# Performance work log

Hardware: AMD Instinct MI355X
Metric: run time of the kernel (lower is better)

Reference implementation:

```python
import jax, jax.numpy as jnp
import numpy as np

B, N, CQ, CKV, CP = 4, 1024, 128, 64, 16
H, NB = 4, 3
D = CQ // H  # 32 per-head dim
NQ, NK = 32, 128
CENTRES = 15.5 + 32.0 * np.arange(N // NQ)  # subset centres covering all atoms


def _ln(x, eps=1e-5):
    m = jnp.mean(x, axis=-1, keepdims=True)
    v = jnp.var(x, axis=-1, keepdims=True)
    return (x - m) * jax.lax.rsqrt(v + eps)


def _adaln(a, s, s_gamma, w_gate, w_skip):
    # AF3 AdaLN: a normalized without affine, modulated by conditioning s
    a_n = _ln(a)
    s_n = _ln(s) * s_gamma
    return jax.nn.sigmoid(s_n @ w_gate) * a_n + s_n @ w_skip


def _local_bias():
    # sequence-local block mask (union over subset centres), Algorithm 7
    idx = jnp.arange(N, dtype=jnp.float32)
    cen = jnp.asarray(CENTRES, dtype=jnp.float32)
    lcond = jnp.abs(idx[None, :] - cen[:, None]) < NQ / 2  # [C, N] query window
    mcond = jnp.abs(idx[None, :] - cen[:, None]) < NK / 2  # [C, N] key window
    cond = jnp.any(lcond[:, :, None] & mcond[:, None, :], axis=0)  # [N, N]
    return jnp.where(cond, 0.0, -1e10)


def _forward(q, c, p, attn_s_gamma, attn_gate_w, attn_skip_w, attn_wq, attn_bq,
             attn_wk, attn_wv, attn_lnz_g, attn_lnz_b, attn_wb, attn_wgate,
             attn_wo, attn_ws_out, attn_bs_out, trans_s_gamma, trans_gate_w,
             trans_skip_w, trans_w1, trans_w2, trans_wout, trans_ws_out,
             trans_bs_out):
    beta = _local_bias()  # [N, N]
    inv_sqrt_d = 1.0 / np.sqrt(D)
    a = q
    for i in range(NB):  # 3 structurally distinct blocks
        # --- AttentionPairBias (AF3 Alg 24) ---
        ah = _adaln(a, c, attn_s_gamma[i], attn_gate_w[i], attn_skip_w[i])
        qh = (ah @ attn_wq[i] + attn_bq[i]).reshape(B, N, H, D)
        kh = (ah @ attn_wk[i]).reshape(B, N, H, D)
        vh = (ah @ attn_wv[i]).reshape(B, N, H, D)
        zb = (_ln(p) * attn_lnz_g[i] + attn_lnz_b[i]) @ attn_wb[i]  # [B,N,N,H]
        bias = jnp.transpose(zb, (0, 3, 1, 2)) + beta[None, None]  # [B,H,N,N]
        scores = jnp.einsum('bqhd,bkhd->bhqk', qh, kh) * inv_sqrt_d + bias
        w = jax.nn.softmax(scores, axis=-1)
        o = jnp.einsum('bhqk,bkhd->bqhd', w, vh)
        g = jax.nn.sigmoid((ah @ attn_wgate[i]).reshape(B, N, H, D))
        o = (g * o).reshape(B, N, CQ) @ attn_wo[i]
        attn_out = jax.nn.sigmoid(c @ attn_ws_out[i] + attn_bs_out[i]) * o
        # --- ConditionedTransitionBlock (AF3 Alg 25, n=2 SwiGLU) ---
        t = _adaln(a, c, trans_s_gamma[i], trans_gate_w[i], trans_skip_w[i])
        bm = jax.nn.silu(t @ trans_w1[i]) * (t @ trans_w2[i])
        t_out = jax.nn.sigmoid(c @ trans_ws_out[i] + trans_bs_out[i]) * (bm @ trans_wout[i])
        # AF3 Alg 23: a <- attn_out + transition(a, s)
        a = attn_out + t_out
    return a


def setup_inputs() -> dict:
    key = jax.random.key(0)
    ks = iter(jax.random.split(key, 64))

    def rnd(shape, scale=0.02):
        return jax.random.normal(next(ks), shape, dtype=jnp.float32) * scale

    return {
        'q': jax.random.normal(next(ks), (B, N, CQ), dtype=jnp.float32),
        'c': jax.random.normal(next(ks), (B, N, CKV), dtype=jnp.float32),
        'p': jax.random.normal(next(ks), (B, N, N, CP), dtype=jnp.float32),
        'attn_s_gamma': jnp.ones((NB, CKV), jnp.float32),
        'attn_gate_w': rnd((NB, CKV, CQ)),
        'attn_skip_w': rnd((NB, CKV, CQ)),
        'attn_wq': rnd((NB, CQ, CQ)),
        'attn_bq': jnp.zeros((NB, CQ), jnp.float32),
        'attn_wk': rnd((NB, CQ, CQ)),
        'attn_wv': rnd((NB, CQ, CQ)),
        'attn_lnz_g': jnp.ones((NB, CP), jnp.float32),
        'attn_lnz_b': jnp.zeros((NB, CP), jnp.float32),
        'attn_wb': rnd((NB, CP, H)),
        'attn_wgate': rnd((NB, CQ, CQ)),
        'attn_wo': rnd((NB, CQ, CQ)),
        'attn_ws_out': rnd((NB, CKV, CQ)),
        'attn_bs_out': jnp.full((NB, CQ), -2.0, jnp.float32),
        'trans_s_gamma': jnp.ones((NB, CKV), jnp.float32),
        'trans_gate_w': rnd((NB, CKV, CQ)),
        'trans_skip_w': rnd((NB, CKV, CQ)),
        'trans_w1': rnd((NB, CQ, 2 * CQ)),
        'trans_w2': rnd((NB, CQ, 2 * CQ)),
        'trans_wout': rnd((NB, 2 * CQ, CQ)),
        'trans_ws_out': rnd((NB, CKV, CQ)),
        'trans_bs_out': jnp.full((NB, CQ), -2.0, jnp.float32),
    }


def reference(q, c, p, attn_s_gamma, attn_gate_w, attn_skip_w, attn_wq, attn_bq,
              attn_wk, attn_wv, attn_lnz_g, attn_lnz_b, attn_wb, attn_wgate,
              attn_wo, attn_ws_out, attn_bs_out, trans_s_gamma, trans_gate_w,
              trans_skip_w, trans_w1, trans_w2, trans_wout, trans_ws_out,
              trans_bs_out):
    return _forward(q, c, p, attn_s_gamma, attn_gate_w, attn_skip_w, attn_wq,
                    attn_bq, attn_wk, attn_wv, attn_lnz_g, attn_lnz_b, attn_wb,
                    attn_wgate, attn_wo, attn_ws_out, attn_bs_out,
                    trans_s_gamma, trans_gate_w, trans_skip_w, trans_w1,
                    trans_w2, trans_wout, trans_ws_out, trans_bs_out)
```

## Files before the change

kernel.cpp:

```cpp
#include <hip/hip_runtime.h>
#include <math.h>

#define NB_ 3
#define B_ 4
#define N_ 1024
#define CQ_ 128
#define CKV_ 64
#define CP_ 16
#define H_ 4
#define D_ 32
#define R_ (B_*N_)
#define KW_ 128

__device__ __forceinline__ float sigmoidf_(float x) {
    return 1.0f / (1.0f + __expf(-x));
}

#define AN_OFF 0
#define SA_OFF 1056
#define ST_OFF 1600
#define CR_OFF 2144
#define TH_OFF 2688
#define SCR_OFF 3744
#define SMEM_F (3744 + 6336)

__global__ __launch_bounds__(512, 4) void k_pre(
    const float* __restrict__ a, const float* __restrict__ c,
    const float* __restrict__ a_sg, const float* __restrict__ a_gw,
    const float* __restrict__ a_sw, const float* __restrict__ a_wso,
    const float* __restrict__ a_bso,
// ... 135 lines not shown
                const float4 wlo = *(const float4*)(W + (kk + q) * ldw);
                const float4 whi = *(const float4*)(W + (kk + q) * ldw + 4);
                const float xa = ((const float*)&x40)[q];
                const float xb = ((const float*)&x41)[q];
                acc0[0] += xa * wlo.x; acc0[1] += xa * wlo.y;
                acc0[2] += xa * wlo.z; acc0[3] += xa * wlo.w;
                acc0[4] += xa * whi.x; acc0[5] += xa * whi.y;
                acc0[6] += xa * whi.z; acc0[7] += xa * whi.w;
                acc1[0] += xb * wlo.x; acc1[1] += xb * wlo.y;
                acc1[2] += xb * wlo.z; acc1[3] += xb * wlo.w;
                acc1[4] += xb * whi.x; acc1[5] += xb * whi.y;
                acc1[6] += xb * whi.z; acc1[7] += xb * whi.w;
            }
        }
        if (wave < 4) {
            float* dst = (wave == 0 ? qh : wave == 1 ? kh : wave == 2 ? vh : gh);
            if (wave == 3) {
                #pragma unroll
                for (int e = 0; e < 8; e++) {
                    acc0[e] = sigmoidf_(acc0[e]);
                    acc1[e] = sigmoidf_(acc1[e]);
                }
            }
            *(float4*)(dst + (base + r0) * 128 + c0)     = make_float4(acc0[0], acc0[1], acc0[2], acc0[3]);
            *(float4*)(dst + (base + r0) * 128 + c0 + 4) = make_float4(acc0[4], acc0[5], acc0[6], acc0[7]);
            *(float4*)(dst + (base + r1) * 128 + c0)     = make_float4(acc1[0], acc1[1], acc1[2], acc1[3]);
            *(float4*)(dst + (base + r1) * 128 + c0 + 4) = make_float4(acc1[4], acc1[5], acc1[6], acc1[7]);
        } else {
            float* bsc = smem + SCR_OFF + sel2 * 2080;
            *(float4*)(bsc + r0 * 260 + cb)     = make_float4(acc0[0], acc0[1], acc0[2], acc0[3]);
            *(float4*)(bsc + r0 * 260 + cb + 4) = make_float4(acc0[4], acc0[5], acc0[6], acc0[7]);
// ... 1 lines not shown
            *(float4*)(bsc + r1 * 260 + cb + 4) = make_float4(acc1[4], acc1[5], acc1[6], acc1[7]);
        }
    }
    __syncthreads();

    #pragma unroll
    for (int i2 = 0; i2 < 4; i2++) {
        const int e = t + i2 * 512;
        const int r = e >> 8, cc = e & 255;
        const float a1 = smem[SCR_OFF + r * 260 + cc];
        const float a2 = smem[SCR_OFF + 2080 + r * 260 + cc];
        bm[(base + r) * 256 + cc] = a1 * sigmoidf_(a1) * a2;
    }
}

#define C_AN 0
#define C_TH 1056
#define C_SA 2112
#define C_ST 2656
#define C_CR 3200
#define C_SCR 3744
#define C_SMEM (3744 + 8448)

__global__ __launch_bounds__(512, 4) void k_cpre(
    const float* __restrict__ og, float* __restrict__ bmio,
    const float* __restrict__ wo, const float* __restrict__ wout,
    float* __restrict__ asig, float* __restrict__ tsig,
    const float* __restrict__ c,
    const float* __restrict__ a_sg, const float* __restrict__ a_gw,
    const float* __restrict__ a_sw, const float* __restrict__ a_wso,
    const float* __restrict__ a_bso,
    const float* __restrict__ t_sg, const float* __restrict__ t_gw,
    const float* __restrict__ t_sw, const float* __restrict__ t_wso,
    const float* __restrict__ t_bso,
    const float* __restrict__ wq, const float* __restrict__ bq,
    const float* __restrict__ wk, const float* __restrict__ wv,
    const float* __restrict__ wg,
    const float* __restrict__ w1, const float* __restrict__ w2,
    float* __restrict__ qh, float* __restrict__ kh,
    float* __restrict__ vh, float* __restrict__ gh)
{
    __shared__ float smem[C_SMEM];
    const int t = threadIdx.x;
    const int base = blockIdx.x * 8;
    const int wave = t >> 6, lane = t & 63;
    const int ig = lane >> 4, jc = lane & 15;
    const int c0 = jc * 8;
    const int r0 = ig * 2, r1 = r0 + 1;

    const int rloc = wave, li = lane;
    const float cv  = c[(base + rloc) * 64 + li];
    const float sgA = a_sg[li], sgT = t_sg[li];
    const int e1 = t + 512;
    const int br0 = t >> 7,  bc0 = t & 127;
    const int br1 = e1 >> 7, bc1 = e1 & 127;
    const int gidx0 = (base + br0) * 128 + bc0;
    const int gidx1 = (base + br1) * 128 + bc1;
    const float as0 = asig[gidx0], ts0 = tsig[gidx0];
    const float as1 = asig[gidx1], ts1 = tsig[gidx1];

    {
        float acc0[8], acc1[8];
        #pragma unroll
        for (int e = 0; e < 8; e++) { acc0[e] = 0.f; acc1[e] = 0.f; }
        if (wave < 4) {
            const float* W = wo + c0;
            const float* X = og + base * 128;
            const int kbeg = wave * 32;
            for (int kk = kbeg; kk < kbeg + 32; kk += 4) {
                float4 x40 = *(const float4*)(X + r0 * 128 + kk);
                float4 x41 = *(const float4*)(X + r1 * 128 + kk);
                #pragma unroll
                for (int q = 0; q < 4; q++) {
                    const float4 wlo = *(const float4*)(W + (kk + q) * 128);
                    const float4 whi = *(const float4*)(W + (kk + q) * 128 + 4);
                    const float xa = ((const float*)&x40)[q];
                    const float xb = ((const float*)&x41)[q];
                    acc0[0] += xa * wlo.x; acc0[1] += xa * wlo.y;
                    acc0[2] += xa * wlo.z; acc0[3] += xa * wlo.w;
                    acc0[4] += xa * whi.x; acc0[5] += xa * whi.y;
                    acc0[6] += xa * whi.z; acc0[7] += xa * whi.w;
                    acc1[0] += xb * wlo.x; acc1[1] += xb * wlo.y;
                    acc1[2] += xb * wlo.z; acc1[3] += xb * wlo.w;
                    acc1[4] += xb * whi.x; acc1[5] += xb * whi.y;
                    acc1[6] += xb * whi.z; acc1[7] += xb * whi.w;
                }
// ... 10 lines not shown
                    const float4 wlo = *(const float4*)(W + (kk + q) * 128);
                    const float4 whi = *(const float4*)(W + (kk + q) * 128 + 4);
                    const float xa = ((const float*)&x40)[q];
                    const float xb = ((const float*)&x41)[q];
                    acc0[0] += xa * wlo.x; acc0[1] += xa * wlo.y;
                    acc0[2] += xa * wlo.z; acc0[3] += xa * wlo.w;
                    acc0[4] += xa * whi.x; acc0[5] += xa * whi.y;
                    acc0[6] += xa * whi.z; acc0[7] += xa * whi.w;
                    acc1[0] += xb * wlo.x; acc1[1] += xb * wlo.y;
                    acc1[2] += xb * wlo.z; acc1[3] += xb * wlo.w;
                    acc1[4] += xb * whi.x; acc1[5] += xb * whi.y;
                    acc1[6] += xb * whi.z; acc1[7] += xb * whi.w;
                }
            }
        }
        float* sc = smem + C_SCR + wave * 1056;
        *(float4*)(sc + r0 * 132 + c0)     = make_float4(acc0[0], acc0[1], acc0[2], acc0[3]);
        *(float4*)(sc + r0 * 132 + c0 + 4) = make_float4(acc0[4], acc0[5], acc0[6], acc0[7]);
        *(float4*)(sc + r1 * 132 + c0)     = make_float4(acc1[0], acc1[1], acc1[2], acc1[3]);
        *(float4*)(sc + r1 * 132 + c0 + 4) = make_float4(acc1[4], acc1[5], acc1[6], acc1[7]);
    }
    __syncthreads();

    {
        const float* s0 = smem + C_SCR + br0 * 132 + bc0;
        const float so0 = s0[0] + s0[1056] + s0[2112] + s0[3168];
        const float st0 = s0[4224] + s0[5280] + s0[6336] + s0[7392];
        smem[C_AN + br0 * 132 + bc0] = as0 * so0 + ts0 * st0;
        const float* s1 = smem + C_SCR + br1 * 132 + bc1;
        const float so1 = s1[0] + s1[1056] + s1[2112] + s1[3168];
        const float st1 = s1[4224] + s1[5280] + s1[6336] + s1[7392];
        smem[C_AN + br1 * 132 + bc1] = as1 * so1 + ts1 * st1;
    }
    __syncthreads();

    {
        float2 av = *(const float2*)&smem[C_AN + rloc * 132 + li * 2];
        float s = av.x + av.y;
        float ss = av.x * av.x + av.y * av.y;
        float cs = cv, css = cv * cv;
        #pragma unroll
        for (int m = 1; m < 64; m <<= 1) {
            s += __shfl_xor(s, m);
            ss += __shfl_xor(ss, m);
            cs += __shfl_xor(cs, m);
            css += __shfl_xor(css, m);
        }
        const float am = s * (1.0f / 128.0f);
        const float ars = rsqrtf(ss * (1.0f / 128.0f) - am * am + 1e-5f);
        const float cm = cs * (1.0f / 64.0f);
        const float crs = rsqrtf(css * (1.0f / 64.0f) - cm * cm + 1e-5f);
        smem[C_AN + rloc * 132 + li * 2]     = (av.x - am) * ars;
        smem[C_AN + rloc * 132 + li * 2 + 1] = (av.y - am) * ars;
        const float cn = (cv - cm) * crs;
        smem[C_SA + rloc * 68 + li] = cn * sgA;
        smem[C_ST + rloc * 68 + li] = cn * sgT;
        smem[C_CR + rloc * 68 + li] = cv;
    }
    __syncthreads();

    if (wave < 6) {
        const float* W;
        const float* xs;
        switch (wave) {
            case 0: W = a_gw;  xs = smem + C_SA; break;
            case 1: W = a_sw;  xs = smem + C_SA; break;
            case 2: W = t_gw;  xs = smem + C_ST; break;
            case 3: W = t_sw;  xs = smem + C_ST; break;
            case 4: W = a_wso; xs = smem + C_CR; break;
            default: W = t_wso; xs = smem + C_CR; break;
        }
        W += c0;
        float acc0[8], acc1[8];
        #pragma unroll
        for (int e = 0; e < 8; e++) { acc0[e] = 0.f; acc1[e] = 0.f; }
        for (int kk = 0; kk < 64; kk += 4) {
            float4 x40 = *(const float4*)(xs + r0 * 68 + kk);
            float4 x41 = *(const float4*)(xs + r1 * 68 + kk);
            #pragma unroll
            for (int q = 0; q < 4; q++) {
                const float4 wlo = *(const float4*)(W + (kk + q) * 128);
                const float4 whi = *(const float4*)(W + (kk + q) * 128 + 4);
                const float xa = ((const float*)&x40)[q];
                const float xb = ((const float*)&x41)[q];
                acc0[0] += xa * wlo.x; acc0[1] += xa * wlo.y;
                acc0[2] += xa * wlo.z; acc0[3] += xa * wlo.w;
                acc0[4] += xa * whi.x; acc0[5] += xa * whi.y;
                acc0[6] += xa * whi.z; acc0[7] += xa * whi.w;
                acc1[0] += xb * wlo.x; acc1[1] += xb * wlo.y;
                acc1[2] += xb * wlo.z; acc1[3] += xb * wlo.w;
                acc1[4] += xb * whi.x; acc1[5] += xb * whi.y;
                acc1[6] += xb * whi.z; acc1[7] += xb * whi.w;
            }
        }
        float* sc = smem + C_SCR + wave * 1056;
        *(float4*)(sc + r0 * 132 + c0)     = make_float4(acc0[0], acc0[1], acc0[2], acc0[3]);
        *(float4*)(sc + r0 * 132 + c0 + 4) = make_float4(acc0[4], acc0[5], acc0[6], acc0[7]);
        *(float4*)(sc + r1 * 132 + c0)     = make_float4(acc1[0], acc1[1], acc1[2], acc1[3]);
        *(float4*)(sc + r1 * 132 + c0 + 4) = make_float4(acc1[4], acc1[5], acc1[6], acc1[7]);
    }
    __syncthreads();

    #pragma unroll
    for (int i2 = 0; i2 < 2; i2++) {
        const int e = t + i2 * 512;
        const int r = e >> 7, cc = e & 127;
        const float* sc = smem + C_SCR + r * 132 + cc;
        const float anv = smem[C_AN + r * 132 + cc];
        const float ahv = sigmoidf_(sc[0]) * anv + sc[1056];
        const float thv = sigmoidf_(sc[2 * 1056]) * anv + sc[3 * 1056];
        smem[C_AN + r * 132 + cc] = ahv;
        smem[C_TH + r * 132 + cc] = thv;
        const int idx = (base + r) * 128 + cc;
        asig[idx] = sigmoidf_(sc[4 * 1056] + a_bso[cc]);
        tsig[idx] = sigmoidf_(sc[5 * 1056] + t_bso[cc]);
    }
    __syncthreads();

    {
        const float* W;
        const float* xs;
        int ldw, sel2 = 0, cb = 0;
        if (wave < 4) {
            W = (wave == 0 ? wq : wave == 1 ? wk : wave == 2 ? wv : wg) + c0;
            xs = smem + C_AN;
            ldw = 128;
        } else {
            const int u = (wave - 4) * 128 + c0;
            sel2 = u >> 8; cb = u & 255;
            W = (sel2 ? w2 : w1) + cb;
            xs = smem + C_TH;
            ldw = 256;
        }
        float acc0[8], acc1[8];
        #pragma unroll
        for (int e = 0; e < 8; e++) {
            const float init = (wave == 0) ? bq[c0 + e] : 0.f;
            acc0[e] = init; acc1[e] = init;
        }
        for (int kk = 0; kk < 128; kk += 4) {
            float4 x40 = *(const float4*)(xs + r0 * 132 + kk);
            float4 x41 = *(const float4*)(xs + r1 * 132 + kk);
            #pragma unroll
            for (int q = 0; q < 4; q++) {
                const float4 wlo = *(const float4*)(W + (kk + q) * ldw);
                const float4 whi = *(const float4*)(W + (kk + q) * ldw + 4);
                const float xa = ((const float*)&x40)[q];
                const float xb = ((const float*)&x41)[q];
                acc0[0] += xa * wlo.x; acc0[1] += xa * wlo.y;
                acc0[2] += xa * wlo.z; acc0[3] += xa * wlo.w;
                acc0[4] += xa * whi.x; acc0[5] += xa * whi.y;
                acc0[6] += xa * whi.z; acc0[7] += xa * whi.w;
                acc1[0] += xb * wlo.x; acc1[1] += xb * wlo.y;
                acc1[2] += xb * wlo.z; acc1[3] += xb * wlo.w;
                acc1[4] += xb * whi.x; acc1[5] += xb * whi.y;
                acc1[6] += xb * whi.z; acc1[7] += xb * whi.w;
            }
        }
        if (wave < 4) {
            float* dst = (wave == 0 ? qh : wave == 1 ? kh : wave == 2 ? vh : gh);
            if (wave == 3) {
                #pragma unroll
                for (int e = 0; e < 8; e++) {
                    acc0[e] = sigmoidf_(acc0[e]);
                    acc1[e] = sigmoidf_(acc1[e]);
                }
            }
            *(float4*)(dst + (base + r0) * 128 + c0)     = make_float4(acc0[0], acc0[1], acc0[2], acc0[3]);
            *(float4*)(dst + (base + r0) * 128 + c0 + 4) = make_float4(acc0[4], acc0[5], acc0[6], acc0[7]);
            *(float4*)(dst + (base + r1) * 128 + c0)     = make_float4(acc1[0], acc1[1], acc1[2], acc1[3]);
            *(float4*)(dst + (base + r1) * 128 + c0 + 4) = make_float4(acc1[4], acc1[5], acc1[6], acc1[7]);
        } else {
            float* bsc = smem + C_SCR + sel2 * 2080;
            *(float4*)(bsc + r0 * 260 + cb)     = make_float4(acc0[0], acc0[1], acc0[2], acc0[3]);
            *(float4*)(bsc + r0 * 260 + cb + 4) = make_float4(acc0[4], acc0[5], acc0[6], acc0[7]);
            *(float4*)(bsc + r1 * 260 + cb)     = make_float4(acc1[0], acc1[1], acc1[2], acc1[3]);
            *(float4*)(bsc + r1 * 260 + cb + 4) = make_float4(acc1[4], acc1[5], acc1[6], acc1[7]);
        }
    }
    __syncthreads();

    #pragma unroll
    for (int i2 = 0; i2 < 4; i2++) {
        const int e = t + i2 * 512;
        const int r = e >> 8, cc = e & 255;
        const float a1 = smem[C_SCR + r * 260 + cc];
        const float a2 = smem[C_SCR + 2080 + r * 260 + cc];
        bmio[(base + r) * 256 + cc] = a1 * sigmoidf_(a1) * a2;
    }
}

__global__ __launch_bounds__(512, 4) void k_fin(
    const float* __restrict__ og, const float* __restrict__ bm,
    const float* __restrict__ wo, const float* __restrict__ wout,
    const float* __restrict__ asig, const float* __restrict__ tsig,
    float* __restrict__ out)
{
    __shared__ float scr[8 * 1056];
    const int t = threadIdx.x;
    const int base = blockIdx.x * 8;
    const int wave = t >> 6, lane = t & 63;
    const int ig = lane >> 4, jc = lane & 15;
    const int c0 = jc * 8;
    const int r0 = ig * 2, r1 = r0 + 1;

    const int e1 = t + 512;
    const int br0 = t >> 7,  bc0 = t & 127;
    const int br1 = e1 >> 7, bc1 = e1 & 127;
    const int gidx0 = (base + br0) * 128 + bc0;
    const int gidx1 = (base + br1) * 128 + bc1;
    const float as0 = asig[gidx0], ts0 = tsig[gidx0];
    const float as1 = asig[gidx1], ts1 = tsig[gidx1];

    float acc0[8], acc1[8];
    #pragma unroll
    for (int e = 0; e < 8; e++) { acc0[e] = 0.f; acc1[e] = 0.f; }

    if (wave < 4) {
        const float* W = wo + c0;
        const float* X = og + base * 128;
        const int kbeg = wave * 32;
        for (int kk = kbeg; kk < kbeg + 32; kk += 4) {
            float4 x40 = *(const float4*)(X + r0 * 128 + kk);
            float4 x41 = *(const float4*)(X + r1 * 128 + kk);
            #pragma unroll
            for (int q = 0; q < 4; q++) {
                const float4 wlo = *(const float4*)(W + (kk + q) * 128);
                const float4 whi = *(const float4*)(W + (kk + q) * 128 + 4);
                const float xa = ((const float*)&x40)[q];
                const float xb = ((const float*)&x41)[q];
                acc0[0] += xa * wlo.x; acc0[1] += xa * wlo.y;
                acc0[2] += xa * wlo.z; acc0[3] += xa * wlo.w;
                acc0[4] += xa * whi.x; acc0[5] += xa * whi.y;
                acc0[6] += xa * whi.z; acc0[7] += xa * whi.w;
                acc1[0] += xb * wlo.x; acc1[1] += xb * wlo.y;
                acc1[2] += xb * wlo.z; acc1[3] += xb * wlo.w;
                acc1[4] += xb * whi.x; acc1[5] += xb * whi.y;
                acc1[6] += xb * whi.z; acc1[7] += xb * whi.w;
            }
// ... 10 lines not shown
                const float4 wlo = *(const float4*)(W + (kk + q) * 128);
                const float4 whi = *(const float4*)(W + (kk + q) * 128 + 4);
                const float xa = ((const float*)&x40)[q];
                const float xb = ((const float*)&x41)[q];
                acc0[0] += xa * wlo.x; acc0[1] += xa * wlo.y;
                acc0[2] += xa * wlo.z; acc0[3] += xa * wlo.w;
                acc0[4] += xa * whi.x; acc0[5] += xa * whi.y;
                acc0[6] += xa * whi.z; acc0[7] += xa * whi.w;
                acc1[0] += xb * wlo.x; acc1[1] += xb * wlo.y;
                acc1[2] += xb * wlo.z; acc1[3] += xb * wlo.w;
                acc1[4] += xb * whi.x; acc1[5] += xb * whi.y;
                acc1[6] += xb * whi.z; acc1[7] += xb * whi.w;
            }
        }
    }
    float* sc = scr + wave * 1056;
    *(float4*)(sc + r0 * 132 + c0)     = make_float4(acc0[0], acc0[1], acc0[2], acc0[3]);
    *(float4*)(sc + r0 * 132 + c0 + 4) = make_float4(acc0[4], acc0[5], acc0[6], acc0[7]);
    *(float4*)(sc + r1 * 132 + c0)     = make_float4(acc1[0], acc1[1], acc1[2], acc1[3]);
    *(float4*)(sc + r1 * 132 + c0 + 4) = make_float4(acc1[4], acc1[5], acc1[6], acc1[7]);
    __syncthreads();

    {
        const float* s0 = scr + br0 * 132 + bc0;
        out[gidx0] = as0 * (s0[0] + s0[1056] + s0[2112] + s0[3168])
                   + ts0 * (s0[4224] + s0[5280] + s0[6336] + s0[7392]);
        const float* s1 = scr + br1 * 132 + bc1;
        out[gidx1] = as1 * (s1[0] + s1[1056] + s1[2112] + s1[3168])
                   + ts1 * (s1[4224] + s1[5280] + s1[6336] + s1[7392]);
    }
}

__global__ __launch_bounds__(256) void k_zbias(
    const float* __restrict__ p,
    const float* __restrict__ lnz_g, const float* __restrict__ lnz_b,
    const float* __restrict__ wb, float* __restrict__ zb)
{
    const int tid = blockIdx.x * 256 + threadIdx.x;
    const int kk = tid & 127;
    const int n = (tid >> 7) & 1023;
    const int b = tid >> 17;
    const int row = b * N_ + n;
// ... 29 lines not shown
        const float* g = lnz_g + blk * 16;
        const float* bb = lnz_b + blk * 16;
        const float* w = wb + blk * 64;
        float z0 = 0.f, z1 = 0.f, z2 = 0.f, z3 = 0.f;
        #pragma unroll
        for (int cp = 0; cp < 16; cp++) {
            const float val = (pv[cp] - m) * rs * g[cp] + bb[cp];
            z0 += val * w[cp * 4 + 0];
            z1 += val * w[cp * 4 + 1];
            z2 += val * w[cp * 4 + 2];
            z3 += val * w[cp * 4 + 3];
        }
        float* zo = zb + ((size_t)(blk * R_ + row) * H_) * KW_ + kk;
        zo[0] = z0; zo[KW_] = z1; zo[2 * KW_] = z2; zo[3 * KW_] = z3;
    }
}

__global__ __launch_bounds__(256) void k_attn(
    const float* __restrict__ qh, const float* __restrict__ kh,
    const float* __restrict__ vh, const float* __restrict__ gh,
    const float* __restrict__ zb, float* __restrict__ og)
{
    __shared__ float kT[32][136];
    __shared__ float vs[128][36];
    __shared__ float wsm[32][132];

    const int t = threadIdx.x;
    const int qb = blockIdx.x, h = blockIdx.y, b = blockIdx.z;
    const int k0 = qb * 32 - 48;

    #pragma unroll
    for (int i = 0; i < 4; i++) {
        const int e = t + i * 256;
        const int kk = e >> 3, d4 = (e & 7) * 4;
        const int kg = k0 + kk;
        float4 kv = make_float4(0.f, 0.f, 0.f, 0.f);
        float4 vv = make_float4(0.f, 0.f, 0.f, 0.f);
        if (kg >= 0 && kg < N_) {
            const int addr = (b * N_ + kg) * 128 + h * 32 + d4;
            kv = *(const float4*)(kh + addr);
            vv = *(const float4*)(vh + addr);
        }
        kT[d4 + 0][kk] = kv.x;
        kT[d4 + 1][kk] = kv.y;
        kT[d4 + 2][kk] = kv.z;
        kT[d4 + 3][kk] = kv.w;
        *(float4*)&vs[kk][d4] = vv;
    }

    const int q = t >> 3, j = t & 7;
    const int n = qb * 32 + q;
    const float* qrow = qh + (b * N_ + n) * 128 + h * 32;
    float4 qf[8];
    #pragma unroll
    for (int dq = 0; dq < 8; dq++) qf[dq] = *(const float4*)(qrow + dq * 4);
    const float* zrow = zb + ((size_t)(b * N_ + n) * H_ + h) * KW_;
    float4 zf[4];
    #pragma unroll
    for (int g4 = 0; g4 < 4; g4++) zf[g4] = *(const float4*)(zrow + g4 * 32 + j * 4);
    __syncthreads();

    float4 acc[4];
    #pragma unroll
    for (int g4 = 0; g4 < 4; g4++) acc[g4] = make_float4(0.f, 0.f, 0.f, 0.f);
    const float* qfs = (const float*)qf;
    #pragma unroll
    for (int d = 0; d < 32; d++) {
        const float qd = qfs[d];
        #pragma unroll
        for (int g4 = 0; g4 < 4; g4++) {
            const float4 k4 = *(const float4*)&kT[d][g4 * 32 + j * 4];
            acc[g4].x += qd * k4.x; acc[g4].y += qd * k4.y;
            acc[g4].z += qd * k4.z; acc[g4].w += qd * k4.w;
        }
    }
    const float scale = 0.1767766952966369f;
    float fr[16];
    #pragma unroll
    for (int g4 = 0; g4 < 4; g4++) {
        fr[g4*4+0] = zf[g4].x + acc[g4].x * scale;
        fr[g4*4+1] = zf[g4].y + acc[g4].y * scale;
        fr[g4*4+2] = zf[g4].z + acc[g4].z * scale;
        fr[g4*4+3] = zf[g4].w + acc[g4].w * scale;
    }
    float mx = fr[0];
    #pragma unroll
    for (int i = 1; i < 16; i++) mx = fmaxf(mx, fr[i]);
    #pragma unroll
    for (int mk = 1; mk < 8; mk <<= 1) mx = fmaxf(mx, __shfl_xor(mx, mk));
    float sum = 0.f;
    #pragma unroll
    for (int i = 0; i < 16; i++) { fr[i] = __expf(fr[i] - mx); sum += fr[i]; }
    #pragma unroll
    for (int mk = 1; mk < 8; mk <<= 1) sum += __shfl_xor(sum, mk);
    const float rinv = 1.0f / sum;
    #pragma unroll
    for (int g4 = 0; g4 < 4; g4++) {
        *(float4*)&wsm[q][g4 * 32 + j * 4] = make_float4(
            fr[g4*4+0] * rinv, fr[g4*4+1] * rinv,
            fr[g4*4+2] * rinv, fr[g4*4+3] * rinv);
    }
    asm volatile("s_waitcnt lgkmcnt(0)" ::: "memory");

    const int addrO = (b * N_ + n) * 128 + h * 32 + j * 4;
    const float4 g4v = *(const float4*)(gh + addrO);
    float4 o = make_float4(0.f, 0.f, 0.f, 0.f);
    #pragma unroll 4
    for (int kk = 0; kk < 128; kk += 4) {
        const float4 w4 = *(const float4*)&wsm[q][kk];
        const float4 v0 = *(const float4*)&vs[kk + 0][j * 4];
        const float4 v1 = *(const float4*)&vs[kk + 1][j * 4];
        const float4 v2 = *(const float4*)&vs[kk + 2][j * 4];
        const float4 v3 = *(const float4*)&vs[kk + 3][j * 4];
        o.x += w4.x * v0.x + w4.y * v1.x + w4.z * v2.x + w4.w * v3.x;
        o.y += w4.x * v0.y + w4.y * v1.y + w4.z * v2.y + w4.w * v3.y;
        o.z += w4.x * v0.z + w4.y * v1.z + w4.z * v2.z + w4.w * v3.z;
        o.w += w4.x * v0.w + w4.y * v1.w + w4.z * v2.w + w4.w * v3.w;
    }
    float4 outv;
    outv.x = o.x * g4v.x; outv.y = o.y * g4v.y;
    outv.z = o.z * g4v.z; outv.w = o.w * g4v.w;
    *(float4*)(og + addrO) = outv;
}

extern "C" void kernel_launch(void* const* d_in, const int* in_sizes, int n_in,
                              void* d_out, int out_size, void* d_ws, size_t ws_size,
                              hipStream_t stream)
{
    const float* q        = (const float*)d_in[0];
    const float* c        = (const float*)d_in[1];
    const float* p        = (const float*)d_in[2];
    const float* a_sg_all = (const float*)d_in[3];
    const float* a_gw_all = (const float*)d_in[4];
    const float* a_sw_all = (const float*)d_in[5];
    const float* wq_all   = (const float*)d_in[6];
    const float* bq_all   = (const float*)d_in[7];
    const float* wk_all   = (const float*)d_in[8];
// ... 4 lines not shown
    const float* wgt_all  = (const float*)d_in[13];
    const float* wo_all   = (const float*)d_in[14];
    const float* awso_all = (const float*)d_in[15];
    const float* abso_all = (const float*)d_in[16];
    const float* t_sg_all = (const float*)d_in[17];
    const float* t_gw_all = (const float*)d_in[18];
    const float* t_sw_all = (const float*)d_in[19];
    const float* w1_all   = (const float*)d_in[20];
    const float* w2_all   = (const float*)d_in[21];
    const float* wout_all = (const float*)d_in[22];
    const float* twso_all = (const float*)d_in[23];
    const float* tbso_all = (const float*)d_in[24];

    float* ws = (float*)d_ws;
    const size_t RC = (size_t)R_ * CQ_;
    float* qh   = ws;
    float* kh   = ws + RC;
    float* vh   = ws + 2 * RC;
    float* gh   = ws + 3 * RC;
    float* bmb  = ws + 4 * RC;
    float* asig = ws + 6 * RC;
    float* tsig = ws + 7 * RC;
    float* ogb  = ws + 8 * RC;
    float* zbb  = ws + 9 * RC;

    k_zbias<<<dim3(B_ * N_ * KW_ / 256), dim3(256), 0, stream>>>(
        p, lnzg_all, lnzb_all, wb_all, zbb);

    k_pre<<<dim3(R_ / 8), dim3(512), 0, stream>>>(
        q, c,
        a_sg_all, a_gw_all, a_sw_all, awso_all, abso_all,
        t_sg_all, t_gw_all, t_sw_all, twso_all, tbso_all,
        wq_all, bq_all, wk_all, wv_all, wgt_all,
        w1_all, w2_all,
        qh, kh, vh, gh, bmb, asig, tsig);

    for (int blk = 0; blk < NB_; blk++) {
        k_attn<<<dim3(N_ / 32, H_, B_), dim3(256), 0, stream>>>(
            qh, kh, vh, gh, zbb + (size_t)blk * R_ * H_ * KW_, ogb);
        if (blk < NB_ - 1) {
            const int nx = blk + 1;
            k_cpre<<<dim3(R_ / 8), dim3(512), 0, stream>>>(
                ogb, bmb,
                wo_all + blk * CQ_ * CQ_, wout_all + blk * 2 * CQ_ * CQ_,
                asig, tsig, c,
                a_sg_all + nx * CKV_, a_gw_all + nx * CKV_ * CQ_,
                a_sw_all + nx * CKV_ * CQ_, awso_all + nx * CKV_ * CQ_,
                abso_all + nx * CQ_,
                t_sg_all + nx * CKV_, t_gw_all + nx * CKV_ * CQ_,
                t_sw_all + nx * CKV_ * CQ_, twso_all + nx * CKV_ * CQ_,
                tbso_all + nx * CQ_,
                wq_all + nx * CQ_ * CQ_, bq_all + nx * CQ_,
                wk_all + nx * CQ_ * CQ_, wv_all + nx * CQ_ * CQ_,
                wgt_all + nx * CQ_ * CQ_,
                w1_all + nx * CQ_ * 2 * CQ_, w2_all + nx * CQ_ * 2 * CQ_,
                qh, kh, vh, gh);
        } else {
            k_fin<<<dim3(R_ / 8), dim3(512), 0, stream>>>(
                ogb, bmb,
                wo_all + blk * CQ_ * CQ_, wout_all + blk * 2 * CQ_ * CQ_,
                asig, tsig, (float*)d_out);
        }
    }
}
```

Measured before the change: 582.0 us.

## Fuse local attention into post-attention and next-block pre-projection kernels

Removes the standalone attention kernel and runs attention for each 8-row tile inside the following kernel, which already does the output projection, transition and next-block QKV projection. The gated attention output stays in shared memory instead of round-tripping through global memory, and three kernel launches are dropped. Q/K/V/G buffers are double-buffered so the fused kernel can write the next block's projections while other tiles still read the current ones. The cost is that only one wave of the 512-thread block does attention math, per head in sequence, and each 8-query tile reloads its full 128-key window, so attention parallelism drops and K/V traffic grows about fourfold.

```diff
diff --git a/kernel.cpp b/kernel.cpp
--- a/kernel.cpp
+++ b/kernel.cpp
@@ -14,6 +14,118 @@
 
 __device__ __forceinline__ float sigmoidf_(float x) {
     return 1.0f / (1.0f + __expf(-x));
+}
+
+__device__ __forceinline__ void attn8_(
+    float* __restrict__ kT, float* __restrict__ vs,
+    float* __restrict__ wsm, float* __restrict__ og,
+    const float* __restrict__ qh, const float* __restrict__ kh,
+    const float* __restrict__ vh, const float* __restrict__ gh,
+    const float* __restrict__ zb, const int base, const int t)
+{
+    const int b = base >> 10;
+    const int nq = base & 1023;
+    const int k0 = ((nq >> 5) << 5) - 48;
+    const float scale = 0.1767766952966369f;
+
+    for (int h = 0; h < H_; h++) {
+        #pragma unroll
+        for (int i = 0; i < 2; i++) {
+            const int e = t + i * 512;
+            const int kk = e >> 3, d4 = (e & 7) * 4;
+            const int kg = k0 + kk;
+            float4 kv = make_float4(0.f, 0.f, 0.f, 0.f);
+            float4 vv = make_float4(0.f, 0.f, 0.f, 0.f);
+            if (kg >= 0 && kg < N_) {
+                const int addr = (b * N_ + kg) * 128 + h * 32 + d4;
+                kv = *(const float4*)(kh + addr);
+                vv = *(const float4*)(vh + addr);
+            }
+            kT[(d4 + 0) * 136 + kk] = kv.x;
+            kT[(d4 + 1) * 136 + kk] = kv.y;
+            kT[(d4 + 2) * 136 + kk] = kv.z;
+            kT[(d4 + 3) * 136 + kk] = kv.w;
+            *(float4*)&vs[kk * 36 + d4] = vv;
+        }
+
+        float4 qf[8];
+        float4 zf[4];
+        if (t < 64) {
+            const int q = t >> 3, j = t & 7;
+            const int row = base + q;
+            const float* qrow = qh + row * 128 + h * 32;
+            #pragma unroll
+            for (int dq = 0; dq < 8; dq++) qf[dq] = *(const float4*)(qrow + dq * 4);
+            const float* zrow = zb + ((size_t)row * H_ + h) * KW_;
+            #pragma unroll
+            for (int g4 = 0; g4 < 4; g4++) zf[g4] = *(const float4*)(zrow + g4 * 32 + j * 4);
+        }
+        __syncthreads();
+
+        if (t < 64) {
+            const int q = t >> 3, j = t & 7;
+            const int row = base + q;
+
+            float4 acc[4];
+            #pragma unroll
+            for (int g4 = 0; g4 < 4; g4++) acc[g4] = make_float4(0.f, 0.f, 0.f, 0.f);
+            const float* qfs = (const float*)qf;
+            #pragma unroll
+            for (int d = 0; d < 32; d++) {
+                const float qd = qfs[d];
+                #pragma unroll
+                for (int g4 = 0; g4 < 4; g4++) {
+                    const float4 k4 = *(const float4*)&kT[d * 136 + g4 * 32 + j * 4];
+                    acc[g4].x += qd * k4.x; acc[g4].y += qd * k4.y;
+                    acc[g4].z += qd * k4.z; acc[g4].w += qd * k4.w;
+                }
+            }
+            float fr[16];
+            #pragma unroll
+            for (int g4 = 0; g4 < 4; g4++) {
+                fr[g4*4+0] = zf[g4].x + acc[g4].x * scale;
+                fr[g4*4+1] = zf[g4].y + acc[g4].y * scale;
+                fr[g4*4+2] = zf[g4].z + acc[g4].z * scale;
+                fr[g4*4+3] = zf[g4].w + acc[g4].w * scale;
+            }
+            float mx = fr[0];
+            #pragma unroll
+            for (int i = 1; i < 16; i++) mx = fmaxf(mx, fr[i]);
+            #pragma unroll
+            for (int mk = 1; mk < 8; mk <<= 1) mx = fmaxf(mx, __shfl_xor(mx, mk));
+            float sum = 0.f;
+            #pragma unroll
+            for (int i = 0; i < 16; i++) { fr[i] = __expf(fr[i] - mx); sum += fr[i]; }
+            #pragma unroll
+            for (int mk = 1; mk < 8; mk <<= 1) sum += __shfl_xor(sum, mk);
+            const float rinv = 1.0f / sum;
+            #pragma unroll
+            for (int g4 = 0; g4 < 4; g4++) {
+                *(float4*)&wsm[q * 132 + g4 * 32 + j * 4] = make_float4(
+                    fr[g4*4+0] * rinv, fr[g4*4+1] * rinv,
+                    fr[g4*4+2] * rinv, fr[g4*4+3] * rinv);
+            }
+            asm volatile("s_waitcnt lgkmcnt(0)" ::: "memory");
+
+            const float4 g4v = *(const float4*)(gh + row * 128 + h * 32 + j * 4);
+            float4 o = make_float4(0.f, 0.f, 0.f, 0.f);
+            #pragma unroll 4
+            for (int kk = 0; kk < 128; kk += 4) {
+                const float4 w4 = *(const float4*)&wsm[q * 132 + kk];
+                const float4 v0 = *(const float4*)&vs[(kk + 0) * 36 + j * 4];
+                const float4 v1 = *(const float4*)&vs[(kk + 1) * 36 + j * 4];
+                const float4 v2 = *(const float4*)&vs[(kk + 2) * 36 + j * 4];
+                const float4 v3 = *(const float4*)&vs[(kk + 3) * 36 + j * 4];
+                o.x += w4.x * v0.x + w4.y * v1.x + w4.z * v2.x + w4.w * v3.x;
+                o.y += w4.x * v0.y + w4.y * v1.y + w4.z * v2.y + w4.w * v3.y;
+                o.z += w4.x * v0.z + w4.y * v1.z + w4.z * v2.z + w4.w * v3.z;
+                o.w += w4.x * v0.w + w4.y * v1.w + w4.z * v2.w + w4.w * v3.w;
+            }
+            *(float4*)&og[q * 132 + h * 32 + j * 4] = make_float4(
+                o.x * g4v.x, o.y * g4v.y, o.z * g4v.z, o.w * g4v.w);
+        }
+        __syncthreads();
+    }
 }
 
 #define AN_OFF 0
@@ -179,7 +291,8 @@
             }
         }
         if (wave < 4) {
-            float* dst = (wave == 0 ? qh : wave == 1 ? kh : wave == 2 ? vh : gh);
+            float* dst = (wave == 0 ? qh : wave == 1 ? kh : wave == 2 ? wv == wv ? vh : vh : gh);
+            dst = (wave == 0 ? qh : wave == 1 ? kh : wave == 2 ? vh : gh);
             if (wave == 3) {
                 #pragma unroll
                 for (int e = 0; e < 8; e++) {
@@ -211,16 +324,22 @@
     }
 }
 
-#define C_AN 0
-#define C_TH 1056
-#define C_SA 2112
-#define C_ST 2656
-#define C_CR 3200
-#define C_SCR 3744
-#define C_SMEM (3744 + 8448)
-
-__global__ __launch_bounds__(512, 4) void k_cpre(
-    const float* __restrict__ og, float* __restrict__ bmio,
+#define A_OG 0
+#define A_KT 1056
+#define A_VS 5408
+#define A_WSM 10016
+#define A_AN 1056
+#define A_TH 2112
+#define A_SA 3168
+#define A_ST 3712
+#define A_CR 4256
+#define A_SCR 4800
+#define A_SMEM 13248
+
+__global__ __launch_bounds__(512, 4) void k_acpre(
+    const float* __restrict__ qhA, const float* __restrict__ khA,
+    const float* __restrict__ vhA, const float* __restrict__ ghA,
+    const float* __restrict__ zb, float* __restrict__ bmio,
     const float* __restrict__ wo, const float* __restrict__ wout,
     float* __restrict__ asig, float* __restrict__ tsig,
     const float* __restrict__ c,
@@ -234,10 +353,10 @@
     const float* __restrict__ wk, const float* __restrict__ wv,
     const float* __restrict__ wg,
     const float* __restrict__ w1, const float* __restrict__ w2,
-    float* __restrict__ qh, float* __restrict__ kh,
-    float* __restrict__ vh, float* __restrict__ gh)
+    float* __restrict__ qhB, float* __restrict__ khB,
+    float* __restrict__ vhB, float* __restrict__ ghB)
 {
-    __shared__ float smem[C_SMEM];
+    __shared__ float smem[A_SMEM];
     const int t = threadIdx.x;
     const int base = blockIdx.x * 8;
     const int wave = t >> 6, lane = t & 63;
@@ -256,17 +375,20 @@
     const float as0 = asig[gidx0], ts0 = tsig[gidx0];
     const float as1 = asig[gidx1], ts1 = tsig[gidx1];
 
+    attn8_(smem + A_KT, smem + A_VS, smem + A_WSM, smem + A_OG,
+           qhA, khA, vhA, ghA, zb, base, t);
+
     {
         float acc0[8], acc1[8];
         #pragma unroll
         for (int e = 0; e < 8; e++) { acc0[e] = 0.f; acc1[e] = 0.f; }
         if (wave < 4) {
             const float* W = wo + c0;
-            const float* X = og + base * 128;
+            const float* X = smem + A_OG;
             const int kbeg = wave * 32;
             for (int kk = kbeg; kk < kbeg + 32; kk += 4) {
-                float4 x40 = *(const float4*)(X + r0 * 128 + kk);
-                float4 x41 = *(const float4*)(X + r1 * 128 + kk);
+                float4 x40 = *(const float4*)(X + r0 * 132 + kk);
+                float4 x41 = *(const float4*)(X + r1 * 132 + kk);
                 #pragma unroll
                 for (int q = 0; q < 4; q++) {
                     const float4 wlo = *(const float4*)(W + (kk + q) * 128);
@@ -307,7 +429,7 @@
                 }
             }
         }
-        float* sc = smem + C_SCR + wave * 1056;
+        float* sc = smem + A_SCR + wave * 1056;
         *(float4*)(sc + r0 * 132 + c0)     = make_float4(acc0[0], acc0[1], acc0[2], acc0[3]);
         *(float4*)(sc + r0 * 132 + c0 + 4) = make_float4(acc0[4], acc0[5], acc0[6], acc0[7]);
         *(float4*)(sc + r1 * 132 + c0)     = make_float4(acc1[0], acc1[1], acc1[2], acc1[3]);
@@ -316,19 +438,19 @@
     __syncthreads();
 
     {
-        const float* s0 = smem + C_SCR + br0 * 132 + bc0;
+        const float* s0 = smem + A_SCR + br0 * 132 + bc0;
         const float so0 = s0[0] + s0[1056] + s0[2112] + s0[3168];
         const float st0 = s0[4224] + s0[5280] + s0[6336] + s0[7392];
-        smem[C_AN + br0 * 132 + bc0] = as0 * so0 + ts0 * st0;
-        const float* s1 = smem + C_SCR + br1 * 132 + bc1;
+        smem[A_AN + br0 * 132 + bc0] = as0 * so0 + ts0 * st0;
+        const float* s1 = smem + A_SCR + br1 * 132 + bc1;
         const float so1 = s1[0] + s1[1056] + s1[2112] + s1[3168];
         const float st1 = s1[4224] + s1[5280] + s1[6336] + s1[7392];
-        smem[C_AN + br1 * 132 + bc1] = as1 * so1 + ts1 * st1;
+        smem[A_AN + br1 * 132 + bc1] = as1 * so1 + ts1 * st1;
     }
     __syncthreads();
 
     {
-        float2 av = *(const float2*)&smem[C_AN + rloc * 132 + li * 2];
+        float2 av = *(const float2*)&smem[A_AN + rloc * 132 + li * 2];
         float s = av.x + av.y;
         float ss = av.x * av.x + av.y * av.y;
         float cs = cv, css = cv * cv;
@@ -343,12 +465,12 @@
         const float ars = rsqrtf(ss * (1.0f / 128.0f) - am * am + 1e-5f);
         const float cm = cs * (1.0f / 64.0f);
         const float crs = rsqrtf(css * (1.0f / 64.0f) - cm * cm + 1e-5f);
-        smem[C_AN + rloc * 132 + li * 2]     = (av.x - am) * ars;
-        smem[C_AN + rloc * 132 + li * 2 + 1] = (av.y - am) * ars;
+        smem[A_AN + rloc * 132 + li * 2]     = (av.x - am) * ars;
+        smem[A_AN + rloc * 132 + li * 2 + 1] = (av.y - am) * ars;
         const float cn = (cv - cm) * crs;
-        smem[C_SA + rloc * 68 + li] = cn * sgA;
-        smem[C_ST + rloc * 68 + li] = cn * sgT;
-        smem[C_CR + rloc * 68 + li] = cv;
+        smem[A_SA + rloc * 68 + li] = cn * sgA;
+        smem[A_ST + rloc * 68 + li] = cn * sgT;
+        smem[A_CR + rloc * 68 + li] = cv;
     }
     __syncthreads();
 
@@ -356,12 +478,12 @@
         const float* W;
         const float* xs;
         switch (wave) {
-            case 0: W = a_gw;  xs = smem + C_SA; break;
-            case 1: W = a_sw;  xs = smem + C_SA; break;
-            case 2: W = t_gw;  xs = smem + C_ST; break;
-            case 3: W = t_sw;  xs = smem + C_ST; break;
-            case 4: W = a_wso; xs = smem + C_CR; break;
-            default: W = t_wso; xs = smem + C_CR; break;
+            case 0: W = a_gw;  xs = smem + A_SA; break;
+            case 1: W = a_sw;  xs = smem + A_SA; break;
+            case 2: W = t_gw;  xs = smem + A_ST; break;
+            case 3: W = t_sw;  xs = smem + A_ST; break;
+            case 4: W = a_wso; xs = smem + A_CR; break;
+            default: W = t_wso; xs = smem + A_CR; break;
         }
         W += c0;
         float acc0[8], acc1[8];
@@ -386,7 +508,7 @@
                 acc1[6] += xb * whi.z; acc1[7] += xb * whi.w;
             }
         }
-        float* sc = smem + C_SCR + wave * 1056;
+        float* sc = smem + A_SCR + wave * 1056;
         *(float4*)(sc + r0 * 132 + c0)     = make_float4(acc0[0], acc0[1], acc0[2], acc0[3]);
         *(float4*)(sc + r0 * 132 + c0 + 4) = make_float4(acc0[4], acc0[5], acc0[6], acc0[7]);
         *(float4*)(sc + r1 * 132 + c0)     = make_float4(acc1[0], acc1[1], acc1[2], acc1[3]);
@@ -398,12 +520,12 @@
     for (int i2 = 0; i2 < 2; i2++) {
         const int e = t + i2 * 512;
         const int r = e >> 7, cc = e & 127;
-        const float* sc = smem + C_SCR + r * 132 + cc;
-        const float anv = smem[C_AN + r * 132 + cc];
+        const float* sc = smem + A_SCR + r * 132 + cc;
+        const float anv = smem[A_AN + r * 132 + cc];
         const float ahv = sigmoidf_(sc[0]) * anv + sc[1056];
         const float thv = sigmoidf_(sc[2 * 1056]) * anv + sc[3 * 1056];
-        smem[C_AN + r * 132 + cc] = ahv;
-        smem[C_TH + r * 132 + cc] = thv;
+        smem[A_AN + r * 132 + cc] = ahv;
+        smem[A_TH + r * 132 + cc] = thv;
         const int idx = (base + r) * 128 + cc;
         asig[idx] = sigmoidf_(sc[4 * 1056] + a_bso[cc]);
         tsig[idx] = sigmoidf_(sc[5 * 1056] + t_bso[cc]);
@@ -416,13 +538,13 @@
         int ldw, sel2 = 0, cb = 0;
         if (wave < 4) {
             W = (wave == 0 ? wq : wave == 1 ? wk : wave == 2 ? wv : wg) + c0;
-            xs = smem + C_AN;
+            xs = smem + A_AN;
             ldw = 128;
         } else {
             const int u = (wave - 4) * 128 + c0;
             sel2 = u >> 8; cb = u & 255;
             W = (sel2 ? w2 : w1) + cb;
-            xs = smem + C_TH;
+            xs = smem + A_TH;
             ldw = 256;
         }
         float acc0[8], acc1[8];
@@ -451,7 +573,7 @@
             }
         }
         if (wave < 4) {
-            float* dst = (wave == 0 ? qh : wave == 1 ? kh : wave == 2 ? vh : gh);
+            float* dst = (wave == 0 ? qhB : wave == 1 ? khB : wave == 2 ? vhB : ghB);
             if (wave == 3) {
                 #pragma unroll
                 for (int e = 0; e < 8; e++) {
@@ -464,7 +586,7 @@
             *(float4*)(dst + (base + r1) * 128 + c0)     = make_float4(acc1[0], acc1[1], acc1[2], acc1[3]);
             *(float4*)(dst + (base + r1) * 128 + c0 + 4) = make_float4(acc1[4], acc1[5], acc1[6], acc1[7]);
         } else {
-            float* bsc = smem + C_SCR + sel2 * 2080;
+            float* bsc = smem + A_SCR + sel2 * 2080;
             *(float4*)(bsc + r0 * 260 + cb)     = make_float4(acc0[0], acc0[1], acc0[2], acc0[3]);
             *(float4*)(bsc + r0 * 260 + cb + 4) = make_float4(acc0[4], acc0[5], acc0[6], acc0[7]);
             *(float4*)(bsc + r1 * 260 + cb)     = make_float4(acc1[0], acc1[1], acc1[2], acc1[3]);
@@ -477,19 +599,28 @@
     for (int i2 = 0; i2 < 4; i2++) {
         const int e = t + i2 * 512;
         const int r = e >> 8, cc = e & 255;
-        const float a1 = smem[C_SCR + r * 260 + cc];
-        const float a2 = smem[C_SCR + 2080 + r * 260 + cc];
+        const float a1 = smem[A_SCR + r * 260 + cc];
+        const float a2 = smem[A_SCR + 2080 + r * 260 + cc];
         bmio[(base + r) * 256 + cc] = a1 * sigmoidf_(a1) * a2;
     }
 }
 
-__global__ __launch_bounds__(512, 4) void k_fin(
-    const float* __restrict__ og, const float* __restrict__ bm,
+#define F_OG 0
+#define F_KT 1056
+#define F_VS 5408
+#define F_WSM 10016
+#define F_SCR 1056
+#define F_SMEM 11072
+
+__global__ __launch_bounds__(512, 4) void k_afin(
+    const float* __restrict__ qhA, const float* __restrict__ khA,
+    const float* __restrict__ vhA, const float* __restrict__ ghA,
+    const float* __restrict__ zb, const float* __restrict__ bm,
     const float* __restrict__ wo, const float* __restrict__ wout,
     const float* __restrict__ asig, const float* __restrict__ tsig,
     float* __restrict__ out)
 {
-    __shared__ float scr[8 * 1056];
+    __shared__ float smem[F_SMEM];
     const int t = threadIdx.x;
     const int base = blockIdx.x * 8;
     const int wave = t >> 6, lane = t & 63;
@@ -505,17 +636,20 @@
     const float as0 = asig[gidx0], ts0 = tsig[gidx0];
     const float as1 = asig[gidx1], ts1 = tsig[gidx1];
 
+    attn8_(smem + F_KT, smem + F_VS, smem + F_WSM, smem + F_OG,
+           qhA, khA, vhA, ghA, zb, base, t);
+
     float acc0[8], acc1[8];
     #pragma unroll
     for (int e = 0; e < 8; e++) { acc0[e] = 0.f; acc1[e] = 0.f; }
 
     if (wave < 4) {
         const float* W = wo + c0;
-        const float* X = og + base * 128;
+        const float* X = smem + F_OG;
         const int kbeg = wave * 32;
         for (int kk = kbeg; kk < kbeg + 32; kk += 4) {
-            float4 x40 = *(const float4*)(X + r0 * 128 + kk);
-            float4 x41 = *(const float4*)(X + r1 * 128 + kk);
+            float4 x40 = *(const float4*)(X + r0 * 132 + kk);
+            float4 x41 = *(const float4*)(X + r1 * 132 + kk);
             #pragma unroll
             for (int q = 0; q < 4; q++) {
                 const float4 wlo = *(const float4*)(W + (kk + q) * 128);
@@ -556,7 +690,7 @@
             }
         }
     }
-    float* sc = scr + wave * 1056;
+    float* sc = smem + F_SCR + wave * 1056;
     *(float4*)(sc + r0 * 132 + c0)     = make_float4(acc0[0], acc0[1], acc0[2], acc0[3]);
     *(float4*)(sc + r0 * 132 + c0 + 4) = make_float4(acc0[4], acc0[5], acc0[6], acc0[7]);
     *(float4*)(sc + r1 * 132 + c0)     = make_float4(acc1[0], acc1[1], acc1[2], acc1[3]);
@@ -564,10 +698,10 @@
     __syncthreads();
 
     {
-        const float* s0 = scr + br0 * 132 + bc0;
+        const float* s0 = smem + F_SCR + br0 * 132 + bc0;
         out[gidx0] = as0 * (s0[0] + s0[1056] + s0[2112] + s0[3168])
                    + ts0 * (s0[4224] + s0[5280] + s0[6336] + s0[7392]);
-        const float* s1 = scr + br1 * 132 + bc1;
+        const float* s1 = smem + F_SCR + br1 * 132 + bc1;
         out[gidx1] = as1 * (s1[0] + s1[1056] + s1[2112] + s1[3168])
                    + ts1 * (s1[4224] + s1[5280] + s1[6336] + s1[7392]);
     }
@@ -627,113 +761,6 @@
         float* zo = zb + ((size_t)(blk * R_ + row) * H_) * KW_ + kk;
         zo[0] = z0; zo[KW_] = z1; zo[2 * KW_] = z2; zo[3 * KW_] = z3;
     }
-}
-
-__global__ __launch_bounds__(256) void k_attn(
-    const float* __restrict__ qh, const float* __restrict__ kh,
-    const float* __restrict__ vh, const float* __restrict__ gh,
-    const float* __restrict__ zb, float* __restrict__ og)
-{
-    __shared__ float kT[32][136];
-    __shared__ float vs[128][36];
-    __shared__ float wsm[32][132];
-
-    const int t = threadIdx.x;
-    const int qb = blockIdx.x, h = blockIdx.y, b = blockIdx.z;
-    const int k0 = qb * 32 - 48;
-
-    #pragma unroll
-    for (int i = 0; i < 4; i++) {
-        const int e = t + i * 256;
-        const int kk = e >> 3, d4 = (e & 7) * 4;
-        const int kg = k0 + kk;
-        float4 kv = make_float4(0.f, 0.f, 0.f, 0.f);
-        float4 vv = make_float4(0.f, 0.f, 0.f, 0.f);
-        if (kg >= 0 && kg < N_) {
-            const int addr = (b * N_ + kg) * 128 + h * 32 + d4;
-            kv = *(const float4*)(kh + addr);
-            vv = *(const float4*)(vh + addr);
-        }
-        kT[d4 + 0][kk] = kv.x;
-        kT[d4 + 1][kk] = kv.y;
-        kT[d4 + 2][kk] = kv.z;
-        kT[d4 + 3][kk] = kv.w;
-        *(float4*)&vs[kk][d4] = vv;
-    }
-
-    const int q = t >> 3, j = t & 7;
-    const int n = qb * 32 + q;
-    const float* qrow = qh + (b * N_ + n) * 128 + h * 32;
-    float4 qf[8];
-    #pragma unroll
-    for (int dq = 0; dq < 8; dq++) qf[dq] = *(const float4*)(qrow + dq * 4);
-    const float* zrow = zb + ((size_t)(b * N_ + n) * H_ + h) * KW_;
-    float4 zf[4];
-    #pragma unroll
-    for (int g4 = 0; g4 < 4; g4++) zf[g4] = *(const float4*)(zrow + g4 * 32 + j * 4);
-    __syncthreads();
-
-    float4 acc[4];
-    #pragma unroll
-    for (int g4 = 0; g4 < 4; g4++) acc[g4] = make_float4(0.f, 0.f, 0.f, 0.f);
-    const float* qfs = (const float*)qf;
-    #pragma unroll
-    for (int d = 0; d < 32; d++) {
-        const float qd = qfs[d];
-        #pragma unroll
-        for (int g4 = 0; g4 < 4; g4++) {
-            const float4 k4 = *(const float4*)&kT[d][g4 * 32 + j * 4];
-            acc[g4].x += qd * k4.x; acc[g4].y += qd * k4.y;
-            acc[g4].z += qd * k4.z; acc[g4].w += qd * k4.w;
-        }
-    }
-    const float scale = 0.1767766952966369f;
-    float fr[16];
-    #pragma unroll
-    for (int g4 = 0; g4 < 4; g4++) {
-        fr[g4*4+0] = zf[g4].x + acc[g4].x * scale;
-        fr[g4*4+1] = zf[g4].y + acc[g4].y * scale;
-        fr[g4*4+2] = zf[g4].z + acc[g4].z * scale;
-        fr[g4*4+3] = zf[g4].w + acc[g4].w * scale;
-    }
-    float mx = fr[0];
-    #pragma unroll
-    for (int i = 1; i < 16; i++) mx = fmaxf(mx, fr[i]);
-    #pragma unroll
-    for (int mk = 1; mk < 8; mk <<= 1) mx = fmaxf(mx, __shfl_xor(mx, mk));
-    float sum = 0.f;
-    #pragma unroll
-    for (int i = 0; i < 16; i++) { fr[i] = __expf(fr[i] - mx); sum += fr[i]; }
-    #pragma unroll
-    for (int mk = 1; mk < 8; mk <<= 1) sum += __shfl_xor(sum, mk);
-    const float rinv = 1.0f / sum;
-    #pragma unroll
-    for (int g4 = 0; g4 < 4; g4++) {
-        *(float4*)&wsm[q][g4 * 32 + j * 4] = make_float4(
-            fr[g4*4+0] * rinv, fr[g4*4+1] * rinv,
-            fr[g4*4+2] * rinv, fr[g4*4+3] * rinv);
-    }
-    asm volatile("s_waitcnt lgkmcnt(0)" ::: "memory");
-
-    const int addrO = (b * N_ + n) * 128 + h * 32 + j * 4;
-    const float4 g4v = *(const float4*)(gh + addrO);
-    float4 o = make_float4(0.f, 0.f, 0.f, 0.f);
-    #pragma unroll 4
-    for (int kk = 0; kk < 128; kk += 4) {
-        const float4 w4 = *(const float4*)&wsm[q][kk];
-        const float4 v0 = *(const float4*)&vs[kk + 0][j * 4];
-        const float4 v1 = *(const float4*)&vs[kk + 1][j * 4];
-        const float4 v2 = *(const float4*)&vs[kk + 2][j * 4];
-        const float4 v3 = *(const float4*)&vs[kk + 3][j * 4];
-        o.x += w4.x * v0.x + w4.y * v1.x + w4.z * v2.x + w4.w * v3.x;
-        o.y += w4.x * v0.y + w4.y * v1.y + w4.z * v2.y + w4.w * v3.y;
-        o.z += w4.x * v0.z + w4.y * v1.z + w4.z * v2.z + w4.w * v3.z;
-        o.w += w4.x * v0.w + w4.y * v1.w + w4.z * v2.w + w4.w * v3.w;
-    }
-    float4 outv;
-    outv.x = o.x * g4v.x; outv.y = o.y * g4v.y;
-    outv.z = o.z * g4v.z; outv.w = o.w * g4v.w;
-    *(float4*)(og + addrO) = outv;
 }
 
 extern "C" void kernel_launch(void* const* d_in, const int* in_sizes, int n_in,
@@ -768,15 +795,20 @@
 
     float* ws = (float*)d_ws;
     const size_t RC = (size_t)R_ * CQ_;
-    float* qh   = ws;
-    float* kh   = ws + RC;
-    float* vh   = ws + 2 * RC;
-    float* gh   = ws + 3 * RC;
-    float* bmb  = ws + 4 * RC;
-    float* asig = ws + 6 * RC;
-    float* tsig = ws + 7 * RC;
-    float* ogb  = ws + 8 * RC;
-    float* zbb  = ws + 9 * RC;
+    float* qh0  = ws;
+    float* kh0  = ws + RC;
+    float* vh0  = ws + 2 * RC;
+    float* gh0  = ws + 3 * RC;
+    float* qh1  = ws + 4 * RC;
+    float* kh1  = ws + 5 * RC;
+    float* vh1  = ws + 6 * RC;
+    float* gh1  = ws + 7 * RC;
+    float* bmb  = ws + 8 * RC;
+    float* asig = ws + 10 * RC;
+    float* tsig = ws + 11 * RC;
+    float* zbb  = ws + 12 * RC;
+
+    const size_t ZL = (size_t)R_ * H_ * KW_;
 
     k_zbias<<<dim3(B_ * N_ * KW_ / 256), dim3(256), 0, stream>>>(
         p, lnzg_all, lnzb_all, wb_all, zbb);
@@ -787,33 +819,40 @@
         t_sg_all, t_gw_all, t_sw_all, twso_all, tbso_all,
         wq_all, bq_all, wk_all, wv_all, wgt_all,
         w1_all, w2_all,
-        qh, kh, vh, gh, bmb, asig, tsig);
-
-    for (int blk = 0; blk < NB_; blk++) {
-        k_attn<<<dim3(N_ / 32, H_, B_), dim3(256), 0, stream>>>(
-            qh, kh, vh, gh, zbb + (size_t)blk * R_ * H_ * KW_, ogb);
-        if (blk < NB_ - 1) {
-            const int nx = blk + 1;
-            k_cpre<<<dim3(R_ / 8), dim3(512), 0, stream>>>(
-                ogb, bmb,
-                wo_all + blk * CQ_ * CQ_, wout_all + blk * 2 * CQ_ * CQ_,
-                asig, tsig, c,
-                a_sg_all + nx * CKV_, a_gw_all + nx * CKV_ * CQ_,
-                a_sw_all + nx * CKV_ * CQ_, awso_all + nx * CKV_ * CQ_,
-                abso_all + nx * CQ_,
-                t_sg_all + nx * CKV_, t_gw_all + nx * CKV_ * CQ_,
-                t_sw_all + nx * CKV_ * CQ_, twso_all + nx * CKV_ * CQ_,
-                tbso_all + nx * CQ_,
-                wq_all + nx * CQ_ * CQ_, bq_all + nx * CQ_,
-                wk_all + nx * CQ_ * CQ_, wv_all + nx * CQ_ * CQ_,
-                wgt_all + nx * CQ_ * CQ_,
-                w1_all + nx * CQ_ * 2 * CQ_, w2_all + nx * CQ_ * 2 * CQ_,
-                qh, kh, vh, gh);
-        } else {
-            k_fin<<<dim3(R_ / 8), dim3(512), 0, stream>>>(
-                ogb, bmb,
-                wo_all + blk * CQ_ * CQ_, wout_all + blk * 2 * CQ_ * CQ_,
-                asig, tsig, (float*)d_out);
-        }
-    }
+        qh0, kh0, vh0, gh0, bmb, asig, tsig);
+
+    k_acpre<<<dim3(R_ / 8), dim3(512), 0, stream>>>(
+        qh0, kh0, vh0, gh0, zbb, bmb,
+        wo_all, wout_all, asig, tsig, c,
+        a_sg_all + 1 * CKV_, a_gw_all + 1 * CKV_ * CQ_,
+        a_sw_all + 1 * CKV_ * CQ_, awso_all + 1 * CKV_ * CQ_,
+        abso_all + 1 * CQ_,
+        t_sg_all + 1 * CKV_, t_gw_all + 1 * CKV_ * CQ_,
+        t_sw_all + 1 * CKV_ * CQ_, twso_all + 1 * CKV_ * CQ_,
+        tbso_all + 1 * CQ_,
+        wq_all + 1 * CQ_ * CQ_, bq_all + 1 * CQ_,
+        wk_all + 1 * CQ_ * CQ_, wv_all + 1 * CQ_ * CQ_,
+        wgt_all + 1 * CQ_ * CQ_,
+        w1_all + 1 * CQ_ * 2 * CQ_, w2_all + 1 * CQ_ * 2 * CQ_,
+        qh1, kh1, vh1, gh1);
+
+    k_acpre<<<dim3(R_ / 8), dim3(512), 0, stream>>>(
+        qh1, kh1, vh1, gh1, zbb + ZL, bmb,
+        wo_all + 1 * CQ_ * CQ_, wout_all + 1 * 2 * CQ_ * CQ_, asig, tsig, c,
+        a_sg_all + 2 * CKV_, a_gw_all + 2 * CKV_ * CQ_,
+        a_sw_all + 2 * CKV_ * CQ_, awso_all + 2 * CKV_ * CQ_,
+        abso_all + 2 * CQ_,
+        t_sg_all + 2 * CKV_, t_gw_all + 2 * CKV_ * CQ_,
+        t_sw_all + 2 * CKV_ * CQ_, twso_all + 2 * CKV_ * CQ_,
+        tbso_all + 2 * CQ_,
+        wq_all + 2 * CQ_ * CQ_, bq_all + 2 * CQ_,
+        wk_all + 2 * CQ_ * CQ_, wv_all + 2 * CQ_ * CQ_,
+        wgt_all + 2 * CQ_ * CQ_,
+        w1_all + 2 * CQ_ * 2 * CQ_, w2_all + 2 * CQ_ * 2 * CQ_,
+        qh0, kh0, vh0, gh0);
+
+    k_afin<<<dim3(R_ / 8), dim3(512), 0, stream>>>(
+        qh0, kh0, vh0, gh0, zbb + 2 * ZL, bmb,
+        wo_all + 2 * CQ_ * CQ_, wout_all + 2 * 2 * CQ_ * CQ_,
+        asig, tsig, (float*)d_out);
 }
```

New measurement: 639.5 us. +9.9%, slower.
